# Performance work log

Hardware: AMD Instinct MI355X
Metric: run time of the kernel (lower is better)

The kernel has to match this reference:

```python
import jax, jax.numpy as jnp
import numpy as np
from jax import lax

INPUT, HIDDEN, LAYERS, ACTIONS = 512, 128, 2, 10
B, T = 512, 256


def _lstm_layer(x_seq, Wih, Whh, bih, bhh):
    """x_seq: [B,T,D] -> (outputs [B,T,H], h_T [B,H], c_T [B,H]). PyTorch gate order i,f,g,o."""
    Bsz = x_seq.shape[0]
    H = Whh.shape[1]
    # Precompute input projection for all timesteps (one big GEMM).
    x_proj = jnp.einsum('btd,gd->btg', x_seq, Wih) + bih + bhh  # [B,T,4H]

    def step(carry, xt):
        h, c = carry
        gates = xt + h @ Whh.T  # [B,4H]
        i, f, g, o = jnp.split(gates, 4, axis=-1)
        c = jax.nn.sigmoid(f) * c + jax.nn.sigmoid(i) * jnp.tanh(g)
        h = jax.nn.sigmoid(o) * jnp.tanh(c)
        return (h, c), h

    init = (jnp.zeros((Bsz, H), x_seq.dtype), jnp.zeros((Bsz, H), x_seq.dtype))
    (hT, cT), hs = lax.scan(step, init, jnp.swapaxes(x_proj, 0, 1))  # hs: [T,B,H]
    return jnp.swapaxes(hs, 0, 1), hT, cT


def setup_inputs() -> dict:
    key = jax.random.key(0)
    ks = jax.random.split(key, 16)
    s_in = 1.0 / np.sqrt(HIDDEN)

    def u(k, shape):
        return jax.random.uniform(k, shape, jnp.float32, -s_in, s_in)

    return {
        'x': jax.random.normal(ks[0], (B, T, INPUT), jnp.float32),
        'Wih0': u(ks[1], (4 * HIDDEN, INPUT)),
        'Whh0': u(ks[2], (4 * HIDDEN, HIDDEN)),
        'bih0': u(ks[3], (4 * HIDDEN,)),
        'bhh0': u(ks[4], (4 * HIDDEN,)),
        'Wih1': u(ks[5], (4 * HIDDEN, HIDDEN)),
        'Whh1': u(ks[6], (4 * HIDDEN, HIDDEN)),
        'bih1': u(ks[7], (4 * HIDDEN,)),
        'bhh1': u(ks[8], (4 * HIDDEN,)),
        'fc1_w': u(ks[9], (HIDDEN // 2, HIDDEN)),
        'fc1_b': u(ks[10], (HIDDEN // 2,)),
        'fc2_w': u(ks[11], (ACTIONS, HIDDEN // 2)),
        'fc2_b': u(ks[12], (ACTIONS,)),
    }


def reference(x, Wih0, Whh0, bih0, bhh0, Wih1, Whh1, bih1, bhh1, fc1_w, fc1_b, fc2_w, fc2_b):
    # Layer 0 (input 512 -> hidden 128); dropout is inference-off (identity).
    h0_seq, h0, c0 = _lstm_layer(x, Wih0, Whh0, bih0, bhh0)
    # Layer 1 (hidden 128 -> hidden 128)
    h1_seq, h1, c1 = _lstm_layer(h0_seq, Wih1, Whh1, bih1, bhh1)
    last = h1_seq[:, -1, :]  # [B,H]
    hid = jax.nn.relu(last @ fc1_w.T + fc1_b)
    logits = hid @ fc2_w.T + fc2_b
    probs = jax.nn.softmax(logits, axis=-1)
    h_n = jnp.stack([h0, h1], axis=0)  # [num_layers,B,H]
    c_n = jnp.stack([c0, c1], axis=0)
    return probs, h_n, c_n
```

## Files before the change

### kernel.cpp

```cpp
#include <hip/hip_runtime.h>
#include <hip/hip_bf16.h>


#define BATCH 512
#define SEQT  256
#define INPUTD 512
#define HID   128
#define GATES 512
#define RB    4
#define SUBS  16

typedef __bf16 bf16_t;
typedef bf16_t bf16x4 __attribute__((ext_vector_type(4)));
typedef bf16_t bf16x8 __attribute__((ext_vector_type(8)));
typedef float  f32x4  __attribute__((ext_vector_type(4)));

__device__ __forceinline__ float sigm(float x) {
    return __builtin_amdgcn_rcpf(1.f + __expf(-x));
}
__device__ __forceinline__ float tanhfast(float x) {
    float xc = fminf(fmaxf(x, -15.f), 15.f);
    float e = __expf(2.f * xc);
    return (e - 1.f) * __builtin_amdgcn_rcpf(e + 1.f);
}

__global__ __launch_bounds__(256) void cvt_f32_bf16(
    const float* __restrict__ in, bf16_t* __restrict__ out, long n4)
{
    long i = (long)blockIdx.x * 256 + threadIdx.x;
    long stride = (long)gridDim.x * 256;
    for (; i < n4; i += stride) {
        float4 v = ((const float4*)in)[i];
        bf16x4 r;
        r[0] = (bf16_t)v.x; r[1] = (bf16_t)v.y;
        r[2] = (bf16_t)v.z; r[3] = (bf16_t)v.w;
        ((bf16x4*)out)[i] = r;
    }
}

__global__ __launch_bounds__(256) void gemm_mfma(
    const bf16_t* __restrict__ A, const bf16_t* __restrict__ W,
    const float* __restrict__ b1, const float* __restrict__ b2,
    float* __restrict__ out,
    int K, int tcs, int tcmask, int srcT, int t0)
{
    __shared__ bf16_t As[128 * 32];
    __shared__ bf16_t Bs[128 * 32];
    int tid = threadIdx.x;
    int l = tid & 63;
    int w = tid >> 6;
    int wm = w >> 1, wn = w & 1;
    int bn = blockIdx.x;
    int bm = blockIdx.y;
    int Tc = tcmask + 1;

    long aoff[2], boff[2];
    #pragma unroll
    for (int c = 0; c < 2; ++c) {
        int m = bm * 128 + (tid >> 2) + 64 * c;
        int xr = ((m >> tcs) * srcT) + t0 + (m & tcmask);
        aoff[c] = (long)xr * K + (tid & 3) * 8;
        int n = bn * 128 + (tid >> 2) + 64 * c;
        boff[c] = (long)n * K + (tid & 3) * 8;
    }

    f32x4 acc[4][4];
    #pragma unroll
    for (int i = 0; i < 4; ++i)
        #pragma unroll
        for (int j = 0; j < 4; ++j)
            acc[i][j] = (f32x4){0.f, 0.f, 0.f, 0.f};

    const int rbase = wm * 64 + (l & 15);
    const int cbase = wn * 64 + (l & 15);
    const int kfrag = (l >> 4) * 8;

    for (int kt = 0; kt < K; kt += 32) {
        __builtin_amdgcn_global_load_lds(
            (const __attribute__((address_space(1))) void*)(A + aoff[0] + kt),
            (__attribute__((address_space(3))) void*)(As + tid * 8), 16, 0, 0);
        __builtin_amdgcn_global_load_lds(
            (const __attribute__((address_space(1))) void*)(A + aoff[1] + kt),
            (__attribute__((address_space(3))) void*)(As + 2048 + tid * 8), 16, 0, 0);
        __builtin_amdgcn_global_load_lds(
            (const __attribute__((address_space(1))) void*)(W + boff[0] + kt),
            (__attribute__((address_space(3))) void*)(Bs + tid * 8), 16, 0, 0);
        __builtin_amdgcn_global_load_lds(
            (const __attribute__((address_space(1))) void*)(W + boff[1] + kt),
            (__attribute__((address_space(3))) void*)(Bs + 2048 + tid * 8), 16, 0, 0);
        __syncthreads();

        bf16x8 af[4], bfr[4];
        #pragma unroll
        for (int i = 0; i < 4; ++i)
            af[i] = *(const bf16x8*)(As + (rbase + i * 16) * 32 + kfrag);
        #pragma unroll
        for (int j = 0; j < 4; ++j)
            bfr[j] = *(const bf16x8*)(Bs + (cbase + j * 16) * 32 + kfrag);

        #pragma unroll
        for (int i = 0; i < 4; ++i)
            #pragma unroll
            for (int j = 0; j < 4; ++j)
                acc[i][j] = __builtin_amdgcn_mfma_f32_16x16x32_bf16(
                    af[i], bfr[j], acc[i][j], 0, 0, 0);
        __syncthreads();
    }

    #pragma unroll
    for (int i = 0; i < 4; ++i) {
        int m0 = bm * 128 + wm * 64 + i * 16 + (l >> 4) * 4;
        #pragma unroll
        for (int j = 0; j < 4; ++j) {
            int n = bn * 128 + wn * 64 + j * 16 + (l & 15);
            float bb = b1[n] + b2[n];
            int hid = n & 127;
            #pragma unroll
            for (int r = 0; r < 4; ++r) {
                int m = m0 + r;
                int b = m >> tcs;
                int t = m & tcmask;
                int br = b >> 2, brow = b & 3;
                out[(((long)br * Tc + t) * 4 + bn) * 512 + brow * 128 + hid] =
                    acc[i][j][r] + bb;
            }
        }
    }
}

#define BARRIER_()                                                             \
    do {                                                                       \
        asm volatile("s_waitcnt lgkmcnt(0)" ::: "memory");                     \
        __builtin_amdgcn_s_barrier();                                          \
        __builtin_amdgcn_sched_barrier(0);                                     \
    } while (0)

#define REC0_STEP(X, t)                                                        \
    {                                                                          \
        bf16x8 a[4];                                                           \
        _Pragma("unroll")                                                      \
        for (int ks = 0; ks < 4; ++ks) {                                       \
            int ba = (col * 256 + ks * 64 + lgroup * 16) ^ ((col & 7) << 4);   \
            a[ks] = *(const bf16x8*)((const char*)h_lds + ba);                 \
        }                                                                      \
        f32x4 acc[4];                                                          \
        _Pragma("unroll")                                                      \
        for (int g = 0; g < 4; ++g) acc[g] = (f32x4){0.f, 0.f, 0.f, 0.f};      \
        _Pragma("unroll")                                                      \
        for (int ks = 0; ks < 4; ++ks)                                         \
            _Pragma("unroll")                                                  \
            for (int g = 0; g < 4; ++g)                                        \
                acc[g] = __builtin_amdgcn_mfma_f32_16x16x32_bf16(              \
                    a[ks], __builtin_bit_cast(bf16x8, wreg[g][ks]), acc[g],    \
                    0, 0, 0);                                                  \
        if (lgroup == 0) {                                                     \
            _Pragma("unroll")                                                  \
            for (int r = 0; r < 4; ++r) {                                      \
                f32x4 v;                                                       \
                v[0] = acc[0][r]; v[1] = acc[1][r];                            \
                v[2] = acc[2][r]; v[3] = acc[3][r];                            \
                *(f32x4*)((char*)g_lds + r * 2048 + coff * 16) = v;            \
            }                                                                  \
        }                                                                      \
        BARRIER_();                                                            \
        {                                                                      \
            f32x4 gv = *(const f32x4*)((const char*)g_lds + tid * 16);         \
            float zi = gv[0] + X.x, zf = gv[1] + X.y;                          \
            float zg = gv[2] + X.z, zo = gv[3] + X.w;                          \
            c = sigm(zf) * c + sigm(zi) * tanhfast(zg);                        \
            h = sigm(zo) * tanhfast(c);                                        \
            *(bf16_t*)((char*)h_lds + hba) = (bf16_t)h;                        \
            h0qp[(long)(t) * 512] = (bf16_t)h;                                 \
        }                                                                      \
        if ((t) + 2 < Tc) {                                                    \
            long o = (long)((t) + 2) * 2048;                                   \
            X.x = xpt[o];        X.y = xpt[o + 512];                           \
            X.z = xpt[o + 1024]; X.w = xpt[o + 1536];                          \
        }                                                                      \
        if (((t) & (SUBS - 1)) == SUBS - 1)                                    \
            asm volatile("s_waitcnt vmcnt(0)" ::: "memory");                   \
        BARRIER_();                                                            \
        if ((((t) & (SUBS - 1)) == SUBS - 1) && tid == 0) {                    \
            __threadfence();                                                   \
            __hip_atomic_store(flagp + ((t) >> 4), 1u, __ATOMIC_RELEASE,       \
                               __HIP_MEMORY_SCOPE_AGENT);                      \
        }                                                                      \
    }

__global__ __launch_bounds__(512, 2) void lstm_dual(
    const float* __restrict__ xp4,
    const bf16_t* __restrict__ Wh0,
    const bf16_t* __restrict__ Wi1,
    const bf16_t* __restrict__ Wh1,
    const float* __restrict__ bih1, const float* __restrict__ bhh1,
    bf16_t* __restrict__ h0q,
    unsigned* __restrict__ flags,
    float* __restrict__ h0st, float* __restrict__ c0st,
    float* __restrict__ h1st, float* __restrict__ c1st,
    int Tc, int first, int subbase)
{
    __shared__ __align__(16) char pool[28 * 1024];
    int tid = threadIdx.x;
    int l = tid & 63;
    int wv = tid >> 6;
    int pair = blockIdx.x & 127;
    int r0 = pair * RB;
    int col = l & 15;
    int lgroup = l >> 4;
    int kreg = lgroup * 8;
    int erow = tid >> 7, ehid = tid & 127;
    const int hba = (erow * 256 + ehid * 2) ^ ((erow & 7) << 4);
    unsigned* flagp = flags + pair * (SEQT / SUBS) + subbase;

    if (blockIdx.x < 128) {
        bf16_t* h_lds = (bf16_t*)pool;
        float*  g_lds = (float*)(pool + 4096);
        int coff = wv * 16 + col;

        f32x4 wreg[4][4];
        #pragma unroll
        for (int g = 0; g < 4; ++g)
            #pragma unroll
            for (int ks = 0; ks < 4; ++ks)
                wreg[g][ks] = *(const f32x4*)(Wh0 + (long)(g * 128 + coff) * HID
                                              + ks * 32 + kreg);
        #pragma unroll
        for (int g = 0; g < 4; ++g)
            #pragma unroll
            for (int ks = 0; ks < 4; ++ks)
                asm volatile("" : "+a"(wreg[g][ks]));

        float c = first ? 0.f : c0st[(r0 + erow) * HID + ehid];
        float h = first ? 0.f : h0st[(r0 + erow) * HID + ehid];

        ((float2*)h_lds)[tid & 255] = make_float2(0.f, 0.f);
        __syncthreads();
        *(bf16_t*)((char*)h_lds + hba) = (bf16_t)h;
        __syncthreads();

        const float* xpt = xp4 + (long)pair * Tc * 2048 + tid;
        bf16_t* h0qp = h0q + (long)pair * Tc * 512 + (hba >> 1);
        float4 xA, xB;
        xA.x = xpt[0];    xA.y = xpt[512];
        xA.z = xpt[1024]; xA.w = xpt[1536];
        if (Tc > 1) {
            xB.x = xpt[2048];        xB.y = xpt[2048 + 512];
            xB.z = xpt[2048 + 1024]; xB.w = xpt[2048 + 1536];
        } else {
            xB = make_float4(0.f, 0.f, 0.f, 0.f);
        }

        for (int tt = 0; tt < Tc; tt += 2) {
            REC0_STEP(xA, tt)
            REC0_STEP(xB, tt + 1)
        }

        h0st[(r0 + erow) * HID + ehid] = h;
        c0st[(r0 + erow) * HID + ehid] = c;
    } else {
        bf16_t* h0stg = (bf16_t*)pool;
        bf16_t* h1_lds = (bf16_t*)(pool + 8192);
        float*  g1a = (float*)(pool + 12288);
        float*  g1b = (float*)(pool + 20480);
        int isWi = wv < 4;
        int w4 = wv & 3;
        int coff1 = w4 * 32;

        const bf16_t* Wsrc = isWi ? Wi1 : Wh1;
        f32x4 wreg[2][4][4];
        #pragma unroll
        for (int c2 = 0; c2 < 2; ++c2)
            #pragma unroll
            for (int g = 0; g < 4; ++g)
                #pragma unroll
                for (int ks = 0; ks < 4; ++ks)
                    wreg[c2][g][ks] = *(const f32x4*)(
                        Wsrc + (long)(g * 128 + coff1 + c2 * 16 + col) * HID
                        + ks * 32 + kreg);
        #pragma unroll
        for (int c2 = 0; c2 < 2; ++c2)
            #pragma unroll
            for (int g = 0; g < 4; ++g)
                #pragma unroll
                for (int ks = 0; ks < 4; ++ks)
                    asm volatile("" : "+a"(wreg[c2][g][ks]));

        float4 bias1;
        bias1.x = bih1[ehid]       + bhh1[ehid];
        bias1.y = bih1[128 + ehid] + bhh1[128 + ehid];
        bias1.z = bih1[256 + ehid] + bhh1[256 + ehid];
        bias1.w = bih1[384 + ehid] + bhh1[384 + ehid];

        float c1 = first ? 0.f : c1st[(r0 + erow) * HID + ehid];
        float h1 = first ? 0.f : h1st[(r0 + erow) * HID + ehid];

        ((float2*)pool)[tid] = make_float2(0.f, 0.f);
        ((float2*)pool)[tid + 512] = make_float2(0.f, 0.f);
        ((float2*)(pool + 8192))[tid & 255] = make_float2(0.f, 0.f);
        __syncthreads();
        *(bf16_t*)((char*)h1_lds + hba) = (bf16_t)h1;
        __syncthreads();

        if (wv == 0) {
            while (__hip_atomic_load(flagp, __ATOMIC_ACQUIRE,
                                     __HIP_MEMORY_SCOPE_AGENT) == 0u)
                __builtin_amdgcn_s_sleep(2);
            __builtin_amdgcn_global_load_lds(
                (const __attribute__((address_space(1))) void*)(
                    h0q + (long)pair * Tc * 512 + l * 8),
                (__attribute__((address_space(3))) void*)h0stg, 16, 0, 0);
            asm volatile("s_waitcnt vmcnt(0)" ::: "memory");
        }
        __syncthreads();

        for (int t = 0; t < Tc; ++t) {
            int pw = (t + 1) & 3;
            if (t + 1 < Tc && wv == pw) {
                if (((t + 1) & (SUBS - 1)) == 0) {
                    unsigned* fp = flagp + ((t + 1) >> 4);
                    while (__hip_atomic_load(fp, __ATOMIC_ACQUIRE,
                                             __HIP_MEMORY_SCOPE_AGENT) == 0u)
                        __builtin_amdgcn_s_sleep(2);
                }
                __builtin_amdgcn_global_load_lds(
                    (const __attribute__((address_space(1))) void*)(
                        h0q + ((long)pair * Tc + t + 1) * 512 + l * 8),
                    (__attribute__((address_space(3))) void*)(
                        h0stg + ((t + 1) & 1) * 2048), 16, 0, 0);
            }

            const char* asrc = isWi
                ? (const char*)(h0stg + (t & 1) * 2048)
                : (const char*)h1_lds;
            bf16x8 a[4];
            #pragma unroll
            for (int ks = 0; ks < 4; ++ks) {
                int ba = (col * 256 + ks * 64 + lgroup * 16) ^ ((col & 7) << 4);
                a[ks] = *(const bf16x8*)(asrc + ba);
            }
            float* gdst = isWi ? g1a : g1b;
            #pragma unroll
            for (int c2 = 0; c2 < 2; ++c2) {
                f32x4 acc[4];
                #pragma unroll
                for (int g = 0; g < 4; ++g) acc[g] = (f32x4){0.f, 0.f, 0.f, 0.f};
                #pragma unroll
                for (int ks = 0; ks < 4; ++ks)
                    #pragma unroll
                    for (int g = 0; g < 4; ++g)
                        acc[g] = __builtin_amdgcn_mfma_f32_16x16x32_bf16(
                            a[ks], __builtin_bit_cast(bf16x8, wreg[c2][g][ks]),
                            acc[g], 0, 0, 0);
                if (lgroup == 0) {
                    #pragma unroll
                    for (int r = 0; r < 4; ++r) {
                        f32x4 v;
                        v[0] = acc[0][r]; v[1] = acc[1][r];
                        v[2] = acc[2][r]; v[3] = acc[3][r];
                        *(f32x4*)((char*)gdst + r * 2048 +
                                  (coff1 + c2 * 16 + col) * 16) = v;
                    }
                }
            }
            BARRIER_();

            {
                f32x4 gva = *(const f32x4*)((const char*)g1a + tid * 16);
                f32x4 gvb = *(const f32x4*)((const char*)g1b + tid * 16);
                float zi = gva[0] + gvb[0] + bias1.x;
                float zf = gva[1] + gvb[1] + bias1.y;
                float zg = gva[2] + gvb[2] + bias1.z;
                float zo = gva[3] + gvb[3] + bias1.w;
                c1 = sigm(zf) * c1 + sigm(zi) * tanhfast(zg);
                h1 = sigm(zo) * tanhfast(c1);
                *(bf16_t*)((char*)h1_lds + hba) = (bf16_t)h1;
            }
            if (t + 1 < Tc && wv == pw)
                asm volatile("s_waitcnt vmcnt(0)" ::: "memory");
            BARRIER_();
        }

        h1st[(r0 + erow) * HID + ehid] = h1;
        c1st[(r0 + erow) * HID + ehid] = c1;
    }
}

__global__ __launch_bounds__(128) void fc_head(
    const float* __restrict__ h0st, const float* __restrict__ c0st,
    const float* __restrict__ h1st, const float* __restrict__ c1st,
    const float* __restrict__ fc1w, const float* __restrict__ fc1b,
    const float* __restrict__ fc2w, const float* __restrict__ fc2b,
    float* __restrict__ out)
{
    __shared__ float h1_s[HID];
    __shared__ float hid_s[64];
    __shared__ float log_s[10];
    int t = threadIdx.x;
    int b = blockIdx.x;

    h1_s[t] = h1st[b * HID + t];
    __syncthreads();

    if (t < 64) {
        float a = fc1b[t];
        const float* wrow = fc1w + t * HID;
        #pragma unroll 4
        for (int k = 0; k < HID; ++k) a = fmaf(wrow[k], h1_s[k], a);
        hid_s[t] = fmaxf(a, 0.f);
    }
    __syncthreads();

    if (t < 10) {
        float a = fc2b[t];
        const float* wrow = fc2w + t * 64;
        #pragma unroll 4
        for (int k = 0; k < 64; ++k) a = fmaf(wrow[k], hid_s[k], a);
        log_s[t] = a;
    }
    __syncthreads();

    if (t == 0) {
        float m = log_s[0];
        #pragma unroll
        for (int j = 1; j < 10; ++j) m = fmaxf(m, log_s[j]);
        float e[10];
        float s = 0.f;
        #pragma unroll
        for (int j = 0; j < 10; ++j) { e[j] = __expf(log_s[j] - m); s += e[j]; }
        float inv = __builtin_amdgcn_rcpf(s);
        #pragma unroll
        for (int j = 0; j < 10; ++j) out[b * 10 + j] = e[j] * inv;
    }

    float* hn = out + BATCH * 10;
    float* cn = hn + 2 * BATCH * HID;
    hn[b * HID + t] = h0st[b * HID + t];
    hn[BATCH * HID + b * HID + t] = h1_s[t];
    cn[b * HID + t] = c0st[b * HID + t];
    cn[BATCH * HID + b * HID + t] = c1st[b * HID + t];
}

extern "C" void kernel_launch(void* const* d_in, const int* in_sizes, int n_in,
                              void* d_out, int out_size, void* d_ws, size_t ws_size,
                              hipStream_t stream) {
    const float* x    = (const float*)d_in[0];
    const float* Wih0 = (const float*)d_in[1];
    const float* Whh0 = (const float*)d_in[2];
    const float* bih0 = (const float*)d_in[3];
    const float* bhh0 = (const float*)d_in[4];
    const float* Wih1 = (const float*)d_in[5];
    const float* Whh1 = (const float*)d_in[6];
    const float* bih1 = (const float*)d_in[7];
    const float* bhh1 = (const float*)d_in[8];
    const float* fc1w = (const float*)d_in[9];
    const float* fc1b = (const float*)d_in[10];
    const float* fc2w = (const float*)d_in[11];
    const float* fc2b = (const float*)d_in[12];
    float* out = (float*)d_out;

    int Tc = SEQT;
    while (Tc > SUBS) {
        size_t need = (size_t)BATCH * Tc * GATES * 4
                    + (size_t)BATCH * SEQT * INPUTD * 2
                    + ((size_t)GATES * INPUTD + 3 * (size_t)GATES * HID) * 2
                    + (size_t)128 * Tc * 512 * 2
                    + 4 * (size_t)BATCH * HID * 4
                    + 128 * (SEQT / SUBS) * 4 + 512;
        if (need <= ws_size) break;
        Tc >>= 1;
    }
    int tcs = __builtin_ctz((unsigned)Tc);

    float*    xp   = (float*)d_ws;
    bf16_t*   xb   = (bf16_t*)(xp + (size_t)BATCH * Tc * GATES);
    bf16_t*   wb0  = xb + (size_t)BATCH * SEQT * INPUTD;
    bf16_t*   wb1  = wb0 + (size_t)GATES * INPUTD;
    bf16_t*   wh0b = wb1 + (size_t)GATES * HID;
    bf16_t*   wh1b = wh0b + (size_t)GATES * HID;
    bf16_t*   h0q  = wh1b + (size_t)GATES * HID;
    float*    h0st = (float*)(h0q + (size_t)128 * Tc * 512);
    float*    c0st = h0st + (size_t)BATCH * HID;
    float*    h1st = c0st + (size_t)BATCH * HID;
    float*    c1st = h1st + (size_t)BATCH * HID;
    unsigned* flags = (unsigned*)(c1st + (size_t)BATCH * HID);

    hipMemsetAsync(flags, 0, 128 * (SEQT / SUBS) * sizeof(unsigned), stream);

    cvt_f32_bf16<<<2048, 256, 0, stream>>>(x, xb, (long)BATCH * SEQT * INPUTD / 4);
    cvt_f32_bf16<<<256, 256, 0, stream>>>(Wih0, wb0, (long)GATES * INPUTD / 4);
    cvt_f32_bf16<<<64, 256, 0, stream>>>(Wih1, wb1, (long)GATES * HID / 4);
    cvt_f32_bf16<<<64, 256, 0, stream>>>(Whh0, wh0b, (long)GATES * HID / 4);
    cvt_f32_bf16<<<64, 256, 0, stream>>>(Whh1, wh1b, (long)GATES * HID / 4);

    int nchunk = SEQT / Tc;
    dim3 gemm_grid(GATES / 128, (BATCH * Tc) / 128);

    for (int ci = 0; ci < nchunk; ++ci) {
        gemm_mfma<<<gemm_grid, 256, 0, stream>>>(
            xb, wb0, bih0, bhh0, xp, INPUTD, tcs, Tc - 1, SEQT, ci * Tc);
        lstm_dual<<<256, 512, 0, stream>>>(
            xp, wh0b, wb1, wh1b, bih1, bhh1, h0q, flags,
            h0st, c0st, h1st, c1st, Tc, ci == 0, ci * (Tc / SUBS));
    }

    fc_head<<<BATCH, 128, 0, stream>>>(
        h0st, c0st, h1st, c1st, fc1w, fc1b, fc2w, fc2b, out);
}
```

Baseline: 618.7 us.

## Split LSTM recurrences into two interleaved row sets to overlap matmul and gates

Both recurrent layers now treat the 4 batch rows of each block as two independent sets of 2 rows. The MFMA for one set's next step is issued while the other set's waves run the elementwise gate update, so the barrier-separated matmul and activation phases overlap. MFMA sections get raised priority via setprio. Layer 1 now puts both Wi1 and Wh1 fragments in every wave's registers and accumulates them in a single chain, which removes the second gate buffer. Layer-0 flags are kept per set, so layer 1 can start a set as soon as that set's chunk is ready. The four weight-conversion launches are merged into one kernel. The trade-offs are more register pressure, more complex cross-set synchronisation, and twice as many barriers per timestep.

Result: slower. 805.3 us (+30.2%).

```diff
diff --git a/kernel.cpp b/kernel.cpp
--- a/kernel.cpp
+++ b/kernel.cpp
@@ -9,6 +9,7 @@
 #define GATES 512
 #define RB    4
 #define SUBS  16
+#define NCH   (SEQT / SUBS)
 
 typedef __bf16 bf16_t;
 typedef bf16_t bf16x4 __attribute__((ext_vector_type(4)));
@@ -36,6 +37,26 @@
         r[2] = (bf16_t)v.z; r[3] = (bf16_t)v.w;
         ((bf16x4*)out)[i] = r;
     }
+}
+
+__global__ __launch_bounds__(256) void cvt_weights(
+    const float* __restrict__ w0, const float* __restrict__ w1,
+    const float* __restrict__ w2, const float* __restrict__ w3,
+    bf16_t* __restrict__ o0, bf16_t* __restrict__ o1,
+    bf16_t* __restrict__ o2, bf16_t* __restrict__ o3)
+{
+    int b = blockIdx.x;
+    const float* src; bf16_t* dst; long base;
+    if (b < 256)      { src = w0; dst = o0; base = (long)b * 256; }
+    else if (b < 320) { src = w1; dst = o1; base = (long)(b - 256) * 256; }
+    else if (b < 384) { src = w2; dst = o2; base = (long)(b - 320) * 256; }
+    else              { src = w3; dst = o3; base = (long)(b - 384) * 256; }
+    long i = base + threadIdx.x;
+    float4 v = ((const float4*)src)[i];
+    bf16x4 r;
+    r[0] = (bf16_t)v.x; r[1] = (bf16_t)v.y;
+    r[2] = (bf16_t)v.z; r[3] = (bf16_t)v.w;
+    ((bf16x4*)dst)[i] = r;
 }
 
 __global__ __launch_bounds__(256) void gemm_mfma(
@@ -135,7 +156,7 @@
         __builtin_amdgcn_sched_barrier(0);                                     \
     } while (0)
 
-#define REC0_STEP(X, t)                                                        \
+#define PSEG(ACT, TM, EWS, TE, XS, EWVALID)                                    \
     {                                                                          \
         bf16x8 a[4];                                                           \
         _Pragma("unroll")                                                      \
@@ -143,6 +164,7 @@
             int ba = (col * 256 + ks * 64 + lgroup * 16) ^ ((col & 7) << 4);   \
             a[ks] = *(const bf16x8*)((const char*)h_lds + ba);                 \
         }                                                                      \
+        __builtin_amdgcn_s_setprio(1);                                         \
         f32x4 acc[4];                                                          \
         _Pragma("unroll")                                                      \
         for (int g = 0; g < 4; ++g) acc[g] = (f32x4){0.f, 0.f, 0.f, 0.f};      \
@@ -153,38 +175,105 @@
                 acc[g] = __builtin_amdgcn_mfma_f32_16x16x32_bf16(              \
                     a[ks], __builtin_bit_cast(bf16x8, wreg[g][ks]), acc[g],    \
                     0, 0, 0);                                                  \
+        __builtin_amdgcn_s_setprio(0);                                         \
         if (lgroup == 0) {                                                     \
             _Pragma("unroll")                                                  \
-            for (int r = 0; r < 4; ++r) {                                      \
+            for (int j = 0; j < 2; ++j) {                                      \
+                int r = (ACT) * 2 + j;                                         \
                 f32x4 v;                                                       \
                 v[0] = acc[0][r]; v[1] = acc[1][r];                            \
                 v[2] = acc[2][r]; v[3] = acc[3][r];                            \
-                *(f32x4*)((char*)g_lds + r * 2048 + coff * 16) = v;            \
+                *(f32x4*)(gset[ACT] + j * 2048 + coff * 16) = v;               \
             }                                                                  \
         }                                                                      \
-        BARRIER_();                                                            \
-        {                                                                      \
-            f32x4 gv = *(const f32x4*)((const char*)g_lds + tid * 16);         \
-            float zi = gv[0] + X.x, zf = gv[1] + X.y;                          \
-            float zg = gv[2] + X.z, zo = gv[3] + X.w;                          \
+        if ((EWVALID) && myset == (EWS)) {                                     \
+            f32x4 gv = *(const f32x4*)(gset[EWS] + uid * 16);                  \
+            float zi = gv[0] + XS.x, zf = gv[1] + XS.y;                        \
+            float zg = gv[2] + XS.z, zo = gv[3] + XS.w;                        \
             c = sigm(zf) * c + sigm(zi) * tanhfast(zg);                        \
             h = sigm(zo) * tanhfast(c);                                        \
             *(bf16_t*)((char*)h_lds + hba) = (bf16_t)h;                        \
-            h0qp[(long)(t) * 512] = (bf16_t)h;                                 \
-        }                                                                      \
-        if ((t) + 2 < Tc) {                                                    \
-            long o = (long)((t) + 2) * 2048;                                   \
-            X.x = xpt[o];        X.y = xpt[o + 512];                           \
-            X.z = xpt[o + 1024]; X.w = xpt[o + 1536];                          \
-        }                                                                      \
-        if (((t) & (SUBS - 1)) == SUBS - 1)                                    \
+            h0qp[(long)(TE) * 512] = (bf16_t)h;                                \
+            if ((TE) + 2 < Tc) {                                               \
+                long o = (long)((TE) + 2) * 2048;                              \
+                XS.x = xpt[o];        XS.y = xpt[o + 512];                     \
+                XS.z = xpt[o + 1024]; XS.w = xpt[o + 1536];                    \
+            }                                                                  \
+            if (((TE) & 15) == 15)                                             \
+                asm volatile("s_waitcnt vmcnt(0)" ::: "memory");               \
+        }                                                                      \
+        BARRIER_();                                                            \
+        if ((EWVALID) && (((TE) & 15) == 15) && tid == (EWS) * 256) {          \
+            __threadfence();                                                   \
+            __hip_atomic_store(flagp + (EWS) * NCH + subbase + ((TE) >> 4),    \
+                               1u, __ATOMIC_RELEASE, __HIP_MEMORY_SCOPE_AGENT);\
+        }                                                                      \
+    }
+
+#define CSEG(ACT, EWS, EWVALID, DS, DT, DVALID)                                \
+    {                                                                          \
+        if ((DVALID) && wv == 0) {                                             \
+            if (((DT) & 15) == 0) {                                            \
+                unsigned* fp = flagp + (DS) * NCH + subbase + ((DT) >> 4);     \
+                while (__hip_atomic_load(fp, __ATOMIC_ACQUIRE,                 \
+                                         __HIP_MEMORY_SCOPE_AGENT) == 0u)      \
+                    __builtin_amdgcn_s_sleep(2);                               \
+            }                                                                  \
+            if (l < 32)                                                        \
+                __builtin_amdgcn_global_load_lds(                              \
+                    (const __attribute__((address_space(1))) void*)(           \
+                        h0q + ((long)pair * Tc + (DT)) * 512 + (DS) * 256      \
+                        + l * 8),                                              \
+                    (__attribute__((address_space(3))) void*)(                 \
+                        h0stg + (DS) * 256), 16, 0, 0);                        \
+        }                                                                      \
+        bf16x8 a0[4], a1[4];                                                   \
+        _Pragma("unroll")                                                      \
+        for (int ks = 0; ks < 4; ++ks) {                                       \
+            int ba = (col * 256 + ks * 64 + lgroup * 16) ^ ((col & 7) << 4);   \
+            a0[ks] = *(const bf16x8*)((const char*)h0stg + ba);                \
+            a1[ks] = *(const bf16x8*)((const char*)h1_lds + ba);               \
+        }                                                                      \
+        __builtin_amdgcn_s_setprio(1);                                         \
+        f32x4 acc[4];                                                          \
+        _Pragma("unroll")                                                      \
+        for (int g = 0; g < 4; ++g) acc[g] = (f32x4){0.f, 0.f, 0.f, 0.f};      \
+        _Pragma("unroll")                                                      \
+        for (int ks = 0; ks < 4; ++ks)                                         \
+            _Pragma("unroll")                                                  \
+            for (int g = 0; g < 4; ++g)                                        \
+                acc[g] = __builtin_amdgcn_mfma_f32_16x16x32_bf16(              \
+                    a0[ks], __builtin_bit_cast(bf16x8, wI[g][ks]), acc[g],     \
+                    0, 0, 0);                                                  \
+        _Pragma("unroll")                                                      \
+        for (int ks = 0; ks < 4; ++ks)                                         \
+            _Pragma("unroll")                                                  \
+            for (int g = 0; g < 4; ++g)                                        \
+                acc[g] = __builtin_amdgcn_mfma_f32_16x16x32_bf16(              \
+                    a1[ks], __builtin_bit_cast(bf16x8, wH[g][ks]), acc[g],     \
+                    0, 0, 0);                                                  \
+        __builtin_amdgcn_s_setprio(0);                                         \
+        if (lgroup == 0) {                                                     \
+            _Pragma("unroll")                                                  \
+            for (int j = 0; j < 2; ++j) {                                      \
+                int r = (ACT) * 2 + j;                                         \
+                f32x4 v;                                                       \
+                v[0] = acc[0][r]; v[1] = acc[1][r];                            \
+                v[2] = acc[2][r]; v[3] = acc[3][r];                            \
+                *(f32x4*)(gset[ACT] + j * 2048 + coff * 16) = v;               \
+            }                                                                  \
+        }                                                                      \
+        if ((EWVALID) && myset == (EWS)) {                                     \
+            f32x4 gv = *(const f32x4*)(gset[EWS] + uid * 16);                  \
+            float zi = gv[0] + bias1.x, zf = gv[1] + bias1.y;                  \
+            float zg = gv[2] + bias1.z, zo = gv[3] + bias1.w;                  \
+            c = sigm(zf) * c + sigm(zi) * tanhfast(zg);                        \
+            h = sigm(zo) * tanhfast(c);                                        \
+            *(bf16_t*)((char*)h1_lds + hba) = (bf16_t)h;                       \
+        }                                                                      \
+        if (wv == 0)                                                           \
             asm volatile("s_waitcnt vmcnt(0)" ::: "memory");                   \
         BARRIER_();                                                            \
-        if ((((t) & (SUBS - 1)) == SUBS - 1) && tid == 0) {                    \
-            __threadfence();                                                   \
-            __hip_atomic_store(flagp + ((t) >> 4), 1u, __ATOMIC_RELEASE,       \
-                               __HIP_MEMORY_SCOPE_AGENT);                      \
-        }                                                                      \
     }
 
 __global__ __launch_bounds__(512, 2) void lstm_dual(
@@ -199,7 +288,7 @@
     float* __restrict__ h1st, float* __restrict__ c1st,
     int Tc, int first, int subbase)
 {
-    __shared__ __align__(16) char pool[28 * 1024];
+    __shared__ __align__(16) char pool[16 * 1024];
     int tid = threadIdx.x;
     int l = tid & 63;
     int wv = tid >> 6;
@@ -208,14 +297,17 @@
     int col = l & 15;
     int lgroup = l >> 4;
     int kreg = lgroup * 8;
-    int erow = tid >> 7, ehid = tid & 127;
+    int myset = wv >> 2;
+    int uid = tid & 255;
+    int erow = tid >> 7;
+    int ehid = tid & 127;
     const int hba = (erow * 256 + ehid * 2) ^ ((erow & 7) << 4);
-    unsigned* flagp = flags + pair * (SEQT / SUBS) + subbase;
+    unsigned* flagp = flags + pair * 2 * NCH;
+    int coff = wv * 16 + col;
 
     if (blockIdx.x < 128) {
         bf16_t* h_lds = (bf16_t*)pool;
-        float*  g_lds = (float*)(pool + 4096);
-        int coff = wv * 16 + col;
+        char* gset[2] = { pool + 4096, pool + 8192 };
 
         f32x4 wreg[4][4];
         #pragma unroll
@@ -251,39 +343,52 @@
         }
 
         for (int tt = 0; tt < Tc; tt += 2) {
-            REC0_STEP(xA, tt)
-            REC0_STEP(xB, tt + 1)
+            PSEG(0, tt,     1, tt - 1, xB, tt > 0)
+            PSEG(1, tt,     0, tt,     xA, 1)
+            PSEG(0, tt + 1, 1, tt,     xA, 1)
+            PSEG(1, tt + 1, 0, tt + 1, xB, 1)
+        }
+        {
+            if (myset == 1) {
+                f32x4 gv = *(const f32x4*)(gset[1] + uid * 16);
+                float zi = gv[0] + xB.x, zf = gv[1] + xB.y;
+                float zg = gv[2] + xB.z, zo = gv[3] + xB.w;
+                c = sigm(zf) * c + sigm(zi) * tanhfast(zg);
+                h = sigm(zo) * tanhfast(c);
+                h0qp[(long)(Tc - 1) * 512] = (bf16_t)h;
+                asm volatile("s_waitcnt vmcnt(0)" ::: "memory");
+            }
+            BARRIER_();
+            if (tid == 256) {
+                __threadfence();
+                __hip_atomic_store(flagp + NCH + subbase + ((Tc - 1) >> 4), 1u,
+                                   __ATOMIC_RELEASE, __HIP_MEMORY_SCOPE_AGENT);
+            }
         }
 
         h0st[(r0 + erow) * HID + ehid] = h;
         c0st[(r0 + erow) * HID + ehid] = c;
     } else {
-        bf16_t* h0stg = (bf16_t*)pool;
-        bf16_t* h1_lds = (bf16_t*)(pool + 8192);
-        float*  g1a = (float*)(pool + 12288);
-        float*  g1b = (float*)(pool + 20480);
-        int isWi = wv < 4;
-        int w4 = wv & 3;
-        int coff1 = w4 * 32;
-
-        const bf16_t* Wsrc = isWi ? Wi1 : Wh1;
-        f32x4 wreg[2][4][4];
-        #pragma unroll
-        for (int c2 = 0; c2 < 2; ++c2)
+        bf16_t* h0stg  = (bf16_t*)pool;
+        bf16_t* h1_lds = (bf16_t*)(pool + 4096);
+        char* gset[2] = { pool + 8192, pool + 12288 };
+
+        f32x4 wI[4][4], wH[4][4];
+        #pragma unroll
+        for (int g = 0; g < 4; ++g)
             #pragma unroll
-            for (int g = 0; g < 4; ++g)
-                #pragma unroll
-                for (int ks = 0; ks < 4; ++ks)
-                    wreg[c2][g][ks] = *(const f32x4*)(
-                        Wsrc + (long)(g * 128 + coff1 + c2 * 16 + col) * HID
-                        + ks * 32 + kreg);
-        #pragma unroll
-        for (int c2 = 0; c2 < 2; ++c2)
+            for (int ks = 0; ks < 4; ++ks) {
+                long o = (long)(g * 128 + coff) * HID + ks * 32 + kreg;
+                wI[g][ks] = *(const f32x4*)(Wi1 + o);
+                wH[g][ks] = *(const f32x4*)(Wh1 + o);
+            }
+        #pragma unroll
+        for (int g = 0; g < 4; ++g)
             #pragma unroll
-            for (int g = 0; g < 4; ++g)
-                #pragma unroll
-                for (int ks = 0; ks < 4; ++ks)
-                    asm volatile("" : "+a"(wreg[c2][g][ks]));
+            for (int ks = 0; ks < 4; ++ks) {
+                asm volatile("" : "+a"(wI[g][ks]));
+                asm volatile("" : "+a"(wH[g][ks]));
+            }
 
         float4 bias1;
         bias1.x = bih1[ehid]       + bhh1[ehid];
@@ -291,18 +396,22 @@
         bias1.z = bih1[256 + ehid] + bhh1[256 + ehid];
         bias1.w = bih1[384 + ehid] + bhh1[384 + ehid];
 
-        float c1 = first ? 0.f : c1st[(r0 + erow) * HID + ehid];
-        float h1 = first ? 0.f : h1st[(r0 + erow) * HID + ehid];
+        float c = first ? 0.f : c1st[(r0 + erow) * HID + ehid];
+        float h = first ? 0.f : h1st[(r0 + erow) * HID + ehid];
 
         ((float2*)pool)[tid] = make_float2(0.f, 0.f);
         ((float2*)pool)[tid + 512] = make_float2(0.f, 0.f);
-        ((float2*)(pool + 8192))[tid & 255] = make_float2(0.f, 0.f);
-        __syncthreads();
-        *(bf16_t*)((char*)h1_lds + hba) = (bf16_t)h1;
+        __syncthreads();
+        *(bf16_t*)((char*)h1_lds + hba) = (bf16_t)h;
         __syncthreads();
 
         if (wv == 0) {
-            while (__hip_atomic_load(flagp, __ATOMIC_ACQUIRE,
+            unsigned* fp0 = flagp + subbase;
+            while (__hip_atomic_load(fp0, __ATOMIC_ACQUIRE,
+                                     __HIP_MEMORY_SCOPE_AGENT) == 0u)
+                __builtin_amdgcn_s_sleep(2);
+            unsigned* fp1 = flagp + NCH + subbase;
+            while (__hip_atomic_load(fp1, __ATOMIC_ACQUIRE,
                                      __HIP_MEMORY_SCOPE_AGENT) == 0u)
                 __builtin_amdgcn_s_sleep(2);
             __builtin_amdgcn_global_load_lds(
@@ -313,75 +422,22 @@
         }
         __syncthreads();
 
-        for (int t = 0; t < Tc; ++t) {
-            int pw = (t + 1) & 3;
-            if (t + 1 < Tc && wv == pw) {
-                if (((t + 1) & (SUBS - 1)) == 0) {
-                    unsigned* fp = flagp + ((t + 1) >> 4);
-                    while (__hip_atomic_load(fp, __ATOMIC_ACQUIRE,
-                                             __HIP_MEMORY_SCOPE_AGENT) == 0u)
-                        __builtin_amdgcn_s_sleep(2);
-                }
-                __builtin_amdgcn_global_load_lds(
-                    (const __attribute__((address_space(1))) void*)(
-                        h0q + ((long)pair * Tc + t + 1) * 512 + l * 8),
-                    (__attribute__((address_space(3))) void*)(
-                        h0stg + ((t + 1) & 1) * 2048), 16, 0, 0);
-            }
-
-            const char* asrc = isWi
-                ? (const char*)(h0stg + (t & 1) * 2048)
-                : (const char*)h1_lds;
-            bf16x8 a[4];
-            #pragma unroll
-            for (int ks = 0; ks < 4; ++ks) {
-                int ba = (col * 256 + ks * 64 + lgroup * 16) ^ ((col & 7) << 4);
-                a[ks] = *(const bf16x8*)(asrc + ba);
-            }
-            float* gdst = isWi ? g1a : g1b;
-            #pragma unroll
-            for (int c2 = 0; c2 < 2; ++c2) {
-                f32x4 acc[4];
-                #pragma unroll
-                for (int g = 0; g < 4; ++g) acc[g] = (f32x4){0.f, 0.f, 0.f, 0.f};
-                #pragma unroll
-                for (int ks = 0; ks < 4; ++ks)
-                    #pragma unroll
-                    for (int g = 0; g < 4; ++g)
-                        acc[g] = __builtin_amdgcn_mfma_f32_16x16x32_bf16(
-                            a[ks], __builtin_bit_cast(bf16x8, wreg[c2][g][ks]),
-                            acc[g], 0, 0, 0);
-                if (lgroup == 0) {
-                    #pragma unroll
-                    for (int r = 0; r < 4; ++r) {
-                        f32x4 v;
-                        v[0] = acc[0][r]; v[1] = acc[1][r];
-                        v[2] = acc[2][r]; v[3] = acc[3][r];
-                        *(f32x4*)((char*)gdst + r * 2048 +
-                                  (coff1 + c2 * 16 + col) * 16) = v;
-                    }
-                }
-            }
-            BARRIER_();
-
-            {
-                f32x4 gva = *(const f32x4*)((const char*)g1a + tid * 16);
-                f32x4 gvb = *(const f32x4*)((const char*)g1b + tid * 16);
-                float zi = gva[0] + gvb[0] + bias1.x;
-                float zf = gva[1] + gvb[1] + bias1.y;
-                float zg = gva[2] + gvb[2] + bias1.z;
-                float zo = gva[3] + gvb[3] + bias1.w;
-                c1 = sigm(zf) * c1 + sigm(zi) * tanhfast(zg);
-                h1 = sigm(zo) * tanhfast(c1);
-                *(bf16_t*)((char*)h1_lds + hba) = (bf16_t)h1;
-            }
-            if (t + 1 < Tc && wv == pw)
-                asm volatile("s_waitcnt vmcnt(0)" ::: "memory");
-            BARRIER_();
-        }
-
-        h1st[(r0 + erow) * HID + ehid] = h1;
-        c1st[(r0 + erow) * HID + ehid] = c1;
+        for (int tt = 0; tt < Tc; tt += 2) {
+            CSEG(0, 1, tt > 0, 1, tt,     tt > 0)
+            CSEG(1, 0, 1,      0, tt + 1, tt + 1 < Tc)
+            CSEG(0, 1, 1,      1, tt + 1, 1)
+            CSEG(1, 0, 1,      0, tt + 2, tt + 2 < Tc)
+        }
+        if (myset == 1) {
+            f32x4 gv = *(const f32x4*)(gset[1] + uid * 16);
+            float zi = gv[0] + bias1.x, zf = gv[1] + bias1.y;
+            float zg = gv[2] + bias1.z, zo = gv[3] + bias1.w;
+            c = sigm(zf) * c + sigm(zi) * tanhfast(zg);
+            h = sigm(zo) * tanhfast(c);
+        }
+
+        h1st[(r0 + erow) * HID + ehid] = h;
+        c1st[(r0 + erow) * HID + ehid] = c;
     }
 }
 
@@ -465,7 +521,7 @@
                     + ((size_t)GATES * INPUTD + 3 * (size_t)GATES * HID) * 2
                     + (size_t)128 * Tc * 512 * 2
                     + 4 * (size_t)BATCH * HID * 4
-                    + 128 * (SEQT / SUBS) * 4 + 512;
+                    + 128 * 2 * NCH * 4 + 512;
         if (need <= ws_size) break;
         Tc >>= 1;
     }
@@ -484,13 +540,11 @@
     float*    c1st = h1st + (size_t)BATCH * HID;
     unsigned* flags = (unsigned*)(c1st + (size_t)BATCH * HID);
 
-    hipMemsetAsync(flags, 0, 128 * (SEQT / SUBS) * sizeof(unsigned), stream);
+    hipMemsetAsync(flags, 0, 128 * 2 * NCH * sizeof(unsigned), stream);
 
     cvt_f32_bf16<<<2048, 256, 0, stream>>>(x, xb, (long)BATCH * SEQT * INPUTD / 4);
-    cvt_f32_bf16<<<256, 256, 0, stream>>>(Wih0, wb0, (long)GATES * INPUTD / 4);
-    cvt_f32_bf16<<<64, 256, 0, stream>>>(Wih1, wb1, (long)GATES * HID / 4);
-    cvt_f32_bf16<<<64, 256, 0, stream>>>(Whh0, wh0b, (long)GATES * HID / 4);
-    cvt_f32_bf16<<<64, 256, 0, stream>>>(Whh1, wh1b, (long)GATES * HID / 4);
+    cvt_weights<<<448, 256, 0, stream>>>(Wih0, Wih1, Whh0, Whh1,
+                                         wb0, wb1, wh0b, wh1b);
 
     int nchunk = SEQT / Tc;
     dim3 gemm_grid(GATES / 128, (BATCH * Tc) / 128);
```

## Fuse x fp32-to-bf16 conversion into GEMM load and merge weight conversions

Applied to the files above, without the earlier changes.

The GEMM now reads x directly in fp32 from global memory, converts it to bf16 in registers and stores it to LDS. This removes the separate conversion pass over the 256 MB input and its bf16 workspace copy. The four weight conversions and the flag memset are merged into one launch. In exchange, the A-tile load no longer uses the direct global-to-LDS path, and the GEMM reads twice as many bytes for A, with register staging that could expose load latency.

After: 586.7 us. 5.2% less time.

```diff
diff --git a/kernel.cpp b/kernel.cpp
--- a/kernel.cpp
+++ b/kernel.cpp
@@ -9,6 +9,7 @@
 #define GATES 512
 #define RB    4
 #define SUBS  16
+#define NCH   (SEQT / SUBS)
 
 typedef __bf16 bf16_t;
 typedef bf16_t bf16x4 __attribute__((ext_vector_type(4)));
@@ -24,22 +25,36 @@
     return (e - 1.f) * __builtin_amdgcn_rcpf(e + 1.f);
 }
 
-__global__ __launch_bounds__(256) void cvt_f32_bf16(
-    const float* __restrict__ in, bf16_t* __restrict__ out, long n4)
+__global__ __launch_bounds__(256) void cvt_weights(
+    const float* __restrict__ w0, const float* __restrict__ w1,
+    const float* __restrict__ w2, const float* __restrict__ w3,
+    bf16_t* __restrict__ o0, bf16_t* __restrict__ o1,
+    bf16_t* __restrict__ o2, bf16_t* __restrict__ o3,
+    unsigned* __restrict__ flags)
 {
-    long i = (long)blockIdx.x * 256 + threadIdx.x;
-    long stride = (long)gridDim.x * 256;
-    for (; i < n4; i += stride) {
-        float4 v = ((const float4*)in)[i];
-        bf16x4 r;
-        r[0] = (bf16_t)v.x; r[1] = (bf16_t)v.y;
-        r[2] = (bf16_t)v.z; r[3] = (bf16_t)v.w;
-        ((bf16x4*)out)[i] = r;
-    }
+    int b = blockIdx.x;
+    if (b == 448) {
+        uint4 z = make_uint4(0u, 0u, 0u, 0u);
+        #pragma unroll
+        for (int i = 0; i < 4; ++i)
+            ((uint4*)flags)[i * 256 + threadIdx.x] = z;
+        return;
+    }
+    const float* src; bf16_t* dst; long base;
+    if (b < 256)      { src = w0; dst = o0; base = (long)b * 256; }
+    else if (b < 320) { src = w1; dst = o1; base = (long)(b - 256) * 256; }
+    else if (b < 384) { src = w2; dst = o2; base = (long)(b - 320) * 256; }
+    else              { src = w3; dst = o3; base = (long)(b - 384) * 256; }
+    long i = base + threadIdx.x;
+    float4 v = ((const float4*)src)[i];
+    bf16x4 r;
+    r[0] = (bf16_t)v.x; r[1] = (bf16_t)v.y;
+    r[2] = (bf16_t)v.z; r[3] = (bf16_t)v.w;
+    ((bf16x4*)dst)[i] = r;
 }
 
 __global__ __launch_bounds__(256) void gemm_mfma(
-    const bf16_t* __restrict__ A, const bf16_t* __restrict__ W,
+    const float* __restrict__ A, const bf16_t* __restrict__ W,
     const float* __restrict__ b1, const float* __restrict__ b2,
     float* __restrict__ out,
     int K, int tcs, int tcmask, int srcT, int t0)
@@ -76,18 +91,27 @@
     const int kfrag = (l >> 4) * 8;
 
     for (int kt = 0; kt < K; kt += 32) {
-        __builtin_amdgcn_global_load_lds(
-            (const __attribute__((address_space(1))) void*)(A + aoff[0] + kt),
-            (__attribute__((address_space(3))) void*)(As + tid * 8), 16, 0, 0);
-        __builtin_amdgcn_global_load_lds(
-            (const __attribute__((address_space(1))) void*)(A + aoff[1] + kt),
-            (__attribute__((address_space(3))) void*)(As + 2048 + tid * 8), 16, 0, 0);
+        float4 av[2][2];
+        #pragma unroll
+        for (int c = 0; c < 2; ++c) {
+            av[c][0] = *(const float4*)(A + aoff[c] + kt);
+            av[c][1] = *(const float4*)(A + aoff[c] + kt + 4);
+        }
         __builtin_amdgcn_global_load_lds(
             (const __attribute__((address_space(1))) void*)(W + boff[0] + kt),
             (__attribute__((address_space(3))) void*)(Bs + tid * 8), 16, 0, 0);
         __builtin_amdgcn_global_load_lds(
             (const __attribute__((address_space(1))) void*)(W + boff[1] + kt),
             (__attribute__((address_space(3))) void*)(Bs + 2048 + tid * 8), 16, 0, 0);
+        #pragma unroll
+        for (int c = 0; c < 2; ++c) {
+            bf16x8 ab;
+            ab[0] = (bf16_t)av[c][0].x; ab[1] = (bf16_t)av[c][0].y;
+            ab[2] = (bf16_t)av[c][0].z; ab[3] = (bf16_t)av[c][0].w;
+            ab[4] = (bf16_t)av[c][1].x; ab[5] = (bf16_t)av[c][1].y;
+            ab[6] = (bf16_t)av[c][1].z; ab[7] = (bf16_t)av[c][1].w;
+            *(bf16x8*)(As + c * 2048 + tid * 8) = ab;
+        }
         __syncthreads();
 
         bf16x8 af[4], bfr[4];
@@ -210,7 +234,7 @@
     int kreg = lgroup * 8;
     int erow = tid >> 7, ehid = tid & 127;
     const int hba = (erow * 256 + ehid * 2) ^ ((erow & 7) << 4);
-    unsigned* flagp = flags + pair * (SEQT / SUBS) + subbase;
+    unsigned* flagp = flags + pair * NCH + subbase;
 
     if (blockIdx.x < 128) {
         bf16_t* h_lds = (bf16_t*)pool;
@@ -461,19 +485,17 @@
     int Tc = SEQT;
     while (Tc > SUBS) {
         size_t need = (size_t)BATCH * Tc * GATES * 4
-                    + (size_t)BATCH * SEQT * INPUTD * 2
                     + ((size_t)GATES * INPUTD + 3 * (size_t)GATES * HID) * 2
                     + (size_t)128 * Tc * 512 * 2
                     + 4 * (size_t)BATCH * HID * 4
-                    + 128 * (SEQT / SUBS) * 4 + 512;
+                    + 128 * NCH * 4 + 512;
         if (need <= ws_size) break;
         Tc >>= 1;
     }
     int tcs = __builtin_ctz((unsigned)Tc);
 
     float*    xp   = (float*)d_ws;
-    bf16_t*   xb   = (bf16_t*)(xp + (size_t)BATCH * Tc * GATES);
-    bf16_t*   wb0  = xb + (size_t)BATCH * SEQT * INPUTD;
+    bf16_t*   wb0  = (bf16_t*)(xp + (size_t)BATCH * Tc * GATES);
     bf16_t*   wb1  = wb0 + (size_t)GATES * INPUTD;
     bf16_t*   wh0b = wb1 + (size_t)GATES * HID;
     bf16_t*   wh1b = wh0b + (size_t)GATES * HID;
@@ -484,20 +506,15 @@
     float*    c1st = h1st + (size_t)BATCH * HID;
     unsigned* flags = (unsigned*)(c1st + (size_t)BATCH * HID);
 
-    hipMemsetAsync(flags, 0, 128 * (SEQT / SUBS) * sizeof(unsigned), stream);
-
-    cvt_f32_bf16<<<2048, 256, 0, stream>>>(x, xb, (long)BATCH * SEQT * INPUTD / 4);
-    cvt_f32_bf16<<<256, 256, 0, stream>>>(Wih0, wb0, (long)GATES * INPUTD / 4);
-    cvt_f32_bf16<<<64, 256, 0, stream>>>(Wih1, wb1, (long)GATES * HID / 4);
-    cvt_f32_bf16<<<64, 256, 0, stream>>>(Whh0, wh0b, (long)GATES * HID / 4);
-    cvt_f32_bf16<<<64, 256, 0, stream>>>(Whh1, wh1b, (long)GATES * HID / 4);
+    cvt_weights<<<449, 256, 0, stream>>>(Wih0, Wih1, Whh0, Whh1,
+                                         wb0, wb1, wh0b, wh1b, flags);
 
     int nchunk = SEQT / Tc;
     dim3 gemm_grid(GATES / 128, (BATCH * Tc) / 128);
 
     for (int ci = 0; ci < nchunk; ++ci) {
         gemm_mfma<<<gemm_grid, 256, 0, stream>>>(
-            xb, wb0, bih0, bhh0, xp, INPUTD, tcs, Tc - 1, SEQT, ci * Tc);
+            x, wb0, bih0, bhh0, xp, INPUTD, tcs, Tc - 1, SEQT, ci * Tc);
         lstm_dual<<<256, 512, 0, stream>>>(
             xp, wh0b, wb1, wh1b, bih1, bhh1, h0q, flags,
             h0st, c0st, h1st, c1st, Tc, ci == 0, ci * (Tc / SUBS));
```
